# Optimization experiments

Hardware: AMD Instinct MI355X
Metric: run time of the kernel (lower is better)

## Reference

```python
import jax, jax.numpy as jnp
import numpy as np

B, T, DIM, HEADS, KV_HEADS = 2, 2048, 1024, 16, 4
HD = DIM // HEADS  # 64


def _rope(t, sin, cos):
    # interleaved RoPE: pairs (2i, 2i+1) rotated by the same angle
    rot = jnp.stack([-t[..., 1::2], t[..., ::2]], axis=-1).reshape(t.shape)
    return t * cos + rot * sin


def setup_inputs() -> dict:
    key = jax.random.key(0)
    kx, kq, kk, kv, ko = jax.random.split(key, 5)
    x = jax.random.normal(kx, (B, T, DIM), dtype=jnp.float32)
    # standard RoPE tables, [T, HD]
    pos = jnp.arange(T, dtype=jnp.float32)
    inv_freq = 1.0 / (10000.0 ** (jnp.arange(0, HD, 2, dtype=jnp.float32) / HD))
    ang = pos[:, None] * inv_freq[None, :]  # [T, HD/2]
    sin = jnp.repeat(jnp.sin(ang), 2, axis=-1)  # [T, HD]
    cos = jnp.repeat(jnp.cos(ang), 2, axis=-1)
    mask = jnp.ones((B, 1, T), dtype=jnp.float32)  # padding mask (all valid)
    s = 1.0 / np.sqrt(DIM).astype(np.float32)
    Wq = jax.random.normal(kq, (DIM, DIM), dtype=jnp.float32) * s
    Wk = jax.random.normal(kk, (DIM, KV_HEADS * HD), dtype=jnp.float32) * s
    Wv = jax.random.normal(kv, (DIM, KV_HEADS * HD), dtype=jnp.float32) * s
    Wo = jax.random.normal(ko, (DIM, DIM), dtype=jnp.float32) * s
    return {"x": x, "sin": sin, "cos": cos, "mask": mask,
            "Wq": Wq, "Wk": Wk, "Wv": Wv, "Wo": Wo}


def reference(x, sin, cos, mask, Wq, Wk, Wv, Wo):
    Bx, Tx, C = x.shape
    # projections -> [B, H, T, HD] / [B, KV, T, HD]
    q = (x @ Wq).reshape(Bx, Tx, HEADS, HD).transpose(0, 2, 1, 3)
    k = (x @ Wk).reshape(Bx, Tx, KV_HEADS, HD).transpose(0, 2, 1, 3)
    v = (x @ Wv).reshape(Bx, Tx, KV_HEADS, HD).transpose(0, 2, 1, 3)
    # RoPE (sin/cos [T, HD] broadcast over batch/heads)
    q = _rope(q, sin, cos)
    k = _rope(k, sin, cos)
    # GQA: expand kv heads to query heads
    groups = HEADS // KV_HEADS
    k = jnp.repeat(k, groups, axis=1)
    v = jnp.repeat(v, groups, axis=1)
    scores = jnp.einsum('bhqd,bhkd->bhqk', q, k) / np.sqrt(HD).astype(np.float32)
    causal = jnp.tril(jnp.ones((Tx, Tx), dtype=bool))  # [T, T]
    m = (mask[:, None, :, :] > 0) & causal  # [B,1,1,T] & [T,T] -> [B,1,T,T]
    scores = jnp.where(m, scores, jnp.asarray(-1e9, scores.dtype))
    attn = jax.nn.softmax(scores, axis=-1)
    out = jnp.einsum('bhqk,bhkd->bhqd', attn, v)
    out = out.transpose(0, 2, 1, 3).reshape(Bx, Tx, C)
    return out @ Wo
```

## Files before the change

kernel.cpp:

```cpp
#include <hip/hip_runtime.h>
#include <math.h>

typedef __attribute__((ext_vector_type(8))) short bf16x8;
typedef __attribute__((ext_vector_type(4))) float f32x4;
typedef __attribute__((ext_vector_type(4))) unsigned short u16x4;

#define B_    2
#define T_    2048
#define DIM_  1024
#define H_    16
#define KV_   4
#define HD_   64

#define QSCALE 0.1803368801111437f

static __device__ __forceinline__ unsigned short f2bf(float f) {
    union { float f; unsigned int u; } v; v.f = f;
    unsigned int r = v.u + 0x7fff + ((v.u >> 16) & 1);
    return (unsigned short)(r >> 16);
}

static __device__ __forceinline__ unsigned int pkbf(float lo, float hi) {
    union { float f; unsigned int u; } a, b; a.f = lo; b.f = hi;
    return ((a.u + 0x8000u) >> 16) | ((b.u + 0x8000u) & 0xffff0000u);
}

static __device__ __forceinline__ void gload16(const void* g, void* l) {
    __builtin_amdgcn_global_load_lds(
        (const __attribute__((address_space(1))) unsigned int*)g,
        (__attribute__((address_space(3))) unsigned int*)l, 16, 0, 0);
}

#define XB_OFF   0u
#define WT_OFF   4194304u
#define WOT_OFF  5767168u
#define QB_OFF   6815744u
#define KB_OFF   11010048u
#define VTB_OFF  12058624u
#define AB_OFF   13107200u

__global__ __launch_bounds__(256) void cvt_kernel(
    const float* __restrict__ in, unsigned short* __restrict__ out)
{
    const size_t i = ((size_t)blockIdx.x * 256 + threadIdx.x) * 8;
    float4 a = *(const float4*)&in[i];
    float4 b = *(const float4*)&in[i + 4];
    unsigned short u[8] = {f2bf(a.x), f2bf(a.y), f2bf(a.z), f2bf(a.w),
                           f2bf(b.x), f2bf(b.y), f2bf(b.z), f2bf(b.w)};
    *(bf16x8*)&out[i] = *(bf16x8*)u;
}

__global__ __launch_bounds__(256) void wtrans_kernel(
    const float* __restrict__ W, unsigned short* __restrict__ Wt, int N)
{
    __shared__ float Ts[64][65];
    const int n0 = blockIdx.x * 64, k0 = blockIdx.y * 64;
    const int tid = threadIdx.x;
    const int r = tid >> 4, c4 = (tid & 15) * 4;
    #pragma unroll
    for (int i = 0; i < 4; ++i) {
        float4 v = *(const float4*)&W[(size_t)(k0 + r + 16 * i) * N + n0 + c4];
        Ts[r + 16 * i][c4 + 0] = v.x; Ts[r + 16 * i][c4 + 1] = v.y;
        Ts[r + 16 * i][c4 + 2] = v.z; Ts[r + 16 * i][c4 + 3] = v.w;
    }
    __syncthreads();
    const int rn = tid >> 3, ck = (tid & 7) * 8;
    #pragma unroll
    for (int i = 0; i < 2; ++i) {
        int n = rn + 32 * i;
        unsigned short u[8];
        #pragma unroll
        for (int e = 0; e < 8; ++e) u[e] = f2bf(Ts[ck + e][n]);
        *(bf16x8*)&Wt[(size_t)(n0 + n) * 1024 + k0 + ck] = *(bf16x8*)u;
    }
}

__global__ __launch_bounds__(256) void qkv_mfma_kernel(
    const unsigned short* __restrict__ xb, const unsigned short* __restrict__ Wt,
    const float* __restrict__ sinp, const float* __restrict__ cosp,
    unsigned short* __restrict__ Qw, unsigned short* __restrict__ Kw,
    unsigned short* __restrict__ Vtw)
{
    __shared__ __align__(16) unsigned char As[8192];
    __shared__ __align__(16) unsigned char Bs[16384];

    const int tid = threadIdx.x, lane = tid & 63, w = tid >> 6;
    const int lr = lane & 15, lg = lane >> 4;
    const int wm = w >> 1, wn = w & 1;
    const int bn = blockIdx.x, bm = blockIdx.y;
    const int m0 = bm * 64, n0 = bn * 128;

    const int chunkR = lane >> 3;
    const int srcOff = 8 * ((lane & 7) ^ chunkR);

    f32x4 acc[2][4] = {};

    for (int k0 = 0; k0 < 1024; k0 += 64) {
        __syncthreads();
        #pragma unroll
        for (int i = 0; i < 6; ++i) {
            const int c = w * 6 + i;
            if (c < 8) {
                const int row = c * 8 + chunkR;
                gload16(xb + (size_t)(m0 + row) * 1024 + k0 + srcOff, As + c * 1024);
            } else {
                const int row = (c - 8) * 8 + chunkR;
                gload16(Wt + (size_t)(n0 + row) * 1024 + k0 + srcOff,
                        Bs + (c - 8) * 1024);
            }
        }
        __syncthreads();
        #pragma unroll
        for (int kk = 0; kk < 2; ++kk) {
            bf16x8 af[2], bfr[4];
            #pragma unroll
            for (int mf = 0; mf < 2; ++mf) {
                const int row = wm * 32 + mf * 16 + lr;
                af[mf] = *(const bf16x8*)(As + row * 128 +
                          ((kk * 64 + lg * 16) ^ ((row & 7) << 4)));
            }
            #pragma unroll
            for (int nf = 0; nf < 4; ++nf) {
                const int row = wn * 64 + nf * 16 + lr;
                bfr[nf] = *(const bf16x8*)(Bs + row * 128 +
                          ((kk * 64 + lg * 16) ^ ((row & 7) << 4)));
            }
            #pragma unroll
            for (int mf = 0; mf < 2; ++mf)
                #pragma unroll
                for (int nf = 0; nf < 4; ++nf)
                    acc[mf][nf] = __builtin_amdgcn_mfma_f32_16x16x32_bf16(
                        af[mf], bfr[nf], acc[mf][nf], 0, 0, 0);
        }
    }

    const float rsign = (lane & 1) ? 1.f : -1.f;
    #pragma unroll
    for (int nf = 0; nf < 4; ++nf) {
        const int col = n0 + wn * 64 + nf * 16 + lr;
        #pragma unroll
        for (int mf = 0; mf < 2; ++mf) {
            const int mrow = m0 + wm * 32 + mf * 16 + lg * 4;
            const int b = mrow >> 11;
            const int t0 = mrow & 2047;
            if (col < 1280) {
                const int d = col & 63;
                #pragma unroll
                for (int r = 0; r < 4; ++r) {
                    float val = acc[mf][nf][r];
                    float partner = __shfl_xor(val, 1);
                    const int t = t0 + r;
                    float cs = cosp[t * 64 + d], sn = sinp[t * 64 + d];
                    float rv = val * cs + rsign * partner * sn;
                    if (col < 1024) {
                        const int h = col >> 6;
                        Qw[(((size_t)b * H_ + h) * T_ + t) * 64 + d] =
                            f2bf(rv * QSCALE);
                    } else {
                        const int kv = (col - 1024) >> 6;
                        char* krow = (char*)Kw +
                            ((((size_t)b * KV_ + kv) * T_ + t) << 7);
                        *(unsigned short*)(krow + ((2 * d) ^ ((t & 7) << 4))) =
                            f2bf(rv);
                    }
                }
            } else {
                const int cv = col - 1280, kv = cv >> 6, d = cv & 63;
                unsigned short u[4];
                #pragma unroll
                for (int r = 0; r < 4; ++r) u[r] = f2bf(acc[mf][nf][r]);
                char* vrow = (char*)Vtw +
                    ((((size_t)b * KV_ + kv) * 64 + d) * (size_t)T_ * 2);
                *(u16x4*)(vrow + ((2 * t0) ^ ((d & 7) << 4))) = *(u16x4*)u;
            }
        }
    }
}

__global__ __launch_bounds__(512, 4) void attn_kernel(
    const unsigned short* __restrict__ Qg, const unsigned short* __restrict__ Kg,
    const unsigned short* __restrict__ Vtg, const float* __restrict__ maskp,
    unsigned short* __restrict__ attn_out)
{
    __shared__ __align__(16) unsigned char Kl[8192];
    __shared__ __align__(16) unsigned char Vl[8192];
    __shared__ __align__(16) unsigned char Pl[8][2048];
    __shared__ __align__(16) float Ml[2048];

    const int tid  = threadIdx.x;
    const int lane = tid & 63;
    const int w    = tid >> 6;
    const int grp  = w >> 2;
    const int wq   = w & 3;
    const int lr   = lane & 15;
    const int lg   = lane >> 4;

    const int bi   = blockIdx.x;
    const int half = bi >> 8;
    const int j    = bi & 255;
    const int bh   = j >> 3;
    const int idx  = j & 7;
    const int p    = half ? (15 - idx) : idx;
    const int qtA  = 31 - p;
    const int qt   = grp ? p : qtA;
    const int h    = bh & 15;
    const int b    = bh >> 4;
    const int kvh  = h >> 2;
    const int q0   = qt * 64;
    const int qrow = q0 + wq * 16 + lr;

    const char* Kb = (const char*)(Kg  + ((size_t)b * KV_ + kvh) * T_ * HD_);
    const char* Vb = (const char*)(Vtg + ((size_t)b * KV_ + kvh) * HD_ * T_);

    {
        f32x4 mv4 = *(const f32x4*)&maskp[b * T_ + tid * 4];
        f32x4 bv;
        #pragma unroll
        for (int e = 0; e < 4; ++e) bv[e] = mv4[e] > 0.f ? 0.f : -1e30f;
        *(f32x4*)&Ml[tid * 4] = bv;
    }

    const int sr  = lane >> 3;
    const int scb = (lane & 7) * 16;
    unsigned char* Pw = &Pl[w][0];

    const unsigned short* Qbase =
        Qg + (((size_t)b * H_ + h) * T_ + qrow) * HD_;
    const bf16x8 qf0 = *(const bf16x8*)(Qbase + lg * 8);
    const bf16x8 qf1 = *(const bf16x8*)(Qbase + 32 + lg * 8);

    f32x4 o[4] = {};
    float m = -1e30f, l = 0.f;

    for (int kt = 0; kt <= qtA; ++kt) {
        const int k0 = kt * 64;

        {
            const int row = w * 8 + sr;
            gload16(Kb + (size_t)(k0 + row) * 128 + scb, &Kl[w * 1024]);
            gload16(Vb + (size_t)row * 4096 + 2 * k0 + scb, &Vl[w * 1024]);
        }
        __syncthreads();

        if (kt <= qt) {
            f32x4 s[4] = {};
            __builtin_amdgcn_s_setprio(1);
            #pragma unroll
            for (int n = 0; n < 4; ++n) {
                const int key = 16 * n + lr;
                #pragma unroll
                for (int ks = 0; ks < 2; ++ks) {
                    bf16x8 kb = *(const bf16x8*)(Kl +
                        ((key * 128 + 64 * ks + lg * 16) ^ ((key & 7) << 4)));
                    s[n] = __builtin_amdgcn_mfma_f32_16x16x32_bf16(
                        kb, ks == 0 ? qf0 : qf1, s[n], 0, 0, 0);
                }
            }
            __builtin_amdgcn_s_setprio(0);

            if (kt == qt) {
                #pragma unroll
                for (int n = 0; n < 4; ++n) {
                    f32x4 bv = *(const f32x4*)&Ml[k0 + 16 * n + 4 * lg];
                    #pragma unroll
                    for (int r = 0; r < 4; ++r) {
                        const int keyg = k0 + 16 * n + 4 * lg + r;
                        s[n][r] = (keyg <= qrow) ? s[n][r] + bv[r] : -1e30f;
                    }
                }
            } else {
                #pragma unroll
                for (int n = 0; n < 4; ++n) {
                    f32x4 bv = *(const f32x4*)&Ml[k0 + 16 * n + 4 * lg];
                    #pragma unroll
                    for (int r = 0; r < 4; ++r) s[n][r] += bv[r];
                }
            }

            float tmax[4];
            #pragma unroll
            for (int n = 0; n < 4; ++n)
                tmax[n] = fmaxf(fmaxf(s[n][0], s[n][1]), fmaxf(s[n][2], s[n][3]));
            float mx = fmaxf(fmaxf(tmax[0], tmax[1]), fmaxf(tmax[2], tmax[3]));
            mx = fmaxf(mx, __shfl_xor(mx, 16));
            mx = fmaxf(mx, __shfl_xor(mx, 32));
            const float mnew = fmaxf(m, mx);
            const float alpha = exp2f(m - mnew);
            m = mnew;
            #pragma unroll
            for (int n = 0; n < 4; ++n)
                #pragma unroll
                for (int r = 0; r < 4; ++r)
                    s[n][r] = exp2f(s[n][r] - mnew);
            float tsum[4];
            #pragma unroll
            for (int n = 0; n < 4; ++n)
                tsum[n] = (s[n][0] + s[n][1]) + (s[n][2] + s[n][3]);
            float rsum = (tsum[0] + tsum[1]) + (tsum[2] + tsum[3]);
            rsum += __shfl_xor(rsum, 16);
            rsum += __shfl_xor(rsum, 32);
            l = l * alpha + rsum;
            #pragma unroll
            for (int n = 0; n < 4; ++n) o[n] *= alpha;

            #pragma unroll
            for (int n = 0; n < 4; ++n) {
                uint2 wv;
                wv.x = pkbf(s[n][0], s[n][1]);
                wv.y = pkbf(s[n][2], s[n][3]);
                *(uint2*)(Pw + ((lr * 128 + 32 * n + 8 * lg) ^ ((lr & 7) << 4))) = wv;
            }
            bf16x8 pa0 = *(const bf16x8*)(Pw + ((lr * 128 +      lg * 16) ^ ((lr & 7) << 4)));
            bf16x8 pa1 = *(const bf16x8*)(Pw + ((lr * 128 + 64 + lg * 16) ^ ((lr & 7) << 4)));

            __builtin_amdgcn_s_setprio(1);
            #pragma unroll
            for (int n = 0; n < 4; ++n) {
                const int d = 16 * n + lr;
                #pragma unroll
                for (int ks = 0; ks < 2; ++ks) {
                    bf16x8 vb = *(const bf16x8*)(Vl +
                        ((d * 128 + 64 * ks + lg * 16) ^ ((d & 7) << 4)));
                    o[n] = __builtin_amdgcn_mfma_f32_16x16x32_bf16(
                        vb, ks == 0 ? pa0 : pa1, o[n], 0, 0, 0);
                }
            }
            __builtin_amdgcn_s_setprio(0);
        }

        __syncthreads();
    }

    const float linv = 1.f / l;
    unsigned short* orow = attn_out + ((size_t)b * T_ + qrow) * DIM_ + h * HD_;
    #pragma unroll
    for (int n = 0; n < 4; ++n) {
        unsigned short u[4];
        #pragma unroll
        for (int r = 0; r < 4; ++r) u[r] = f2bf(o[n][r] * linv);
        *(u16x4*)&orow[16 * n + 4 * lg] = *(u16x4*)u;
    }
}

__global__ __launch_bounds__(256) void outproj_mfma_kernel(
    const unsigned short* __restrict__ Ab, const unsigned short* __restrict__ Wot,
    float* __restrict__ out)
{
    __shared__ __align__(16) unsigned char As[8192];
    __shared__ __align__(16) unsigned char Bs[16384];

    const int tid = threadIdx.x, lane = tid & 63, w = tid >> 6;
    const int lr = lane & 15, lg = lane >> 4;
    const int wm = w >> 1, wn = w & 1;
    const int bn = blockIdx.x, bm = blockIdx.y;
    const int m0 = bm * 64, n0 = bn * 128;

    const int chunkR = lane >> 3;
    const int srcOff = 8 * ((lane & 7) ^ chunkR);

    f32x4 acc[2][4] = {};

    for (int k0 = 0; k0 < 1024; k0 += 64) {
        __syncthreads();
        #pragma unroll
        for (int i = 0; i < 6; ++i) {
            const int c = w * 6 + i;
            if (c < 8) {
                const int row = c * 8 + chunkR;
                gload16(Ab + (size_t)(m0 + row) * 1024 + k0 + srcOff, As + c * 1024);
            } else {
                const int row = (c - 8) * 8 + chunkR;
                gload16(Wot + (size_t)(n0 + row) * 1024 + k0 + srcOff,
                        Bs + (c - 8) * 1024);
            }
        }
        __syncthreads();
        #pragma unroll
        for (int kk = 0; kk < 2; ++kk) {
            bf16x8 af[2], bfr[4];
            #pragma unroll
            for (int mf = 0; mf < 2; ++mf) {
                const int row = wm * 32 + mf * 16 + lr;
                af[mf] = *(const bf16x8*)(As + row * 128 +
                          ((kk * 64 + lg * 16) ^ ((row & 7) << 4)));
            }
            #pragma unroll
            for (int nf = 0; nf < 4; ++nf) {
                const int row = wn * 64 + nf * 16 + lr;
                bfr[nf] = *(const bf16x8*)(Bs + row * 128 +
                          ((kk * 64 + lg * 16) ^ ((row & 7) << 4)));
            }
            #pragma unroll
            for (int mf = 0; mf < 2; ++mf)
                #pragma unroll
                for (int nf = 0; nf < 4; ++nf)
                    acc[mf][nf] = __builtin_amdgcn_mfma_f32_16x16x32_bf16(
                        af[mf], bfr[nf], acc[mf][nf], 0, 0, 0);
        }
    }

    #pragma unroll
    for (int nf = 0; nf < 4; ++nf) {
        const int col = n0 + wn * 64 + nf * 16 + lr;
        #pragma unroll
        for (int mf = 0; mf < 2; ++mf) {
            const int mrow = m0 + wm * 32 + mf * 16 + lg * 4;
            #pragma unroll
            for (int r = 0; r < 4; ++r)
                out[(size_t)(mrow + r) * 1024 + col] = acc[mf][nf][r];
        }
    }
}

extern "C" void kernel_launch(void* const* d_in, const int* in_sizes, int n_in,
                              void* d_out, int out_size, void* d_ws, size_t ws_size,
                              hipStream_t stream)
{
    const float* x     = (const float*)d_in[0];
    const float* sinp  = (const float*)d_in[1];
    const float* cosp  = (const float*)d_in[2];
    const float* maskp = (const float*)d_in[3];
    const float* Wq    = (const float*)d_in[4];
    const float* Wk    = (const float*)d_in[5];
    const float* Wv    = (const float*)d_in[6];
    const float* Wo    = (const float*)d_in[7];

    unsigned short* wsb = (unsigned short*)d_ws;
    unsigned short* xb  = wsb + XB_OFF;
    unsigned short* Wt  = wsb + WT_OFF;
    unsigned short* Wot = wsb + WOT_OFF;
    unsigned short* Qw  = wsb + QB_OFF;
    unsigned short* Kw  = wsb + KB_OFF;
    unsigned short* Vtw = wsb + VTB_OFF;
    unsigned short* Ab  = wsb + AB_OFF;
    float* out = (float*)d_out;

    cvt_kernel<<<2048, 256, 0, stream>>>(x, xb);
    wtrans_kernel<<<dim3(16, 16), 256, 0, stream>>>(Wq, Wt, 1024);
    wtrans_kernel<<<dim3(4, 16), 256, 0, stream>>>(Wk, Wt + 1024u * 1024u, 256);
    wtrans_kernel<<<dim3(4, 16), 256, 0, stream>>>(Wv, Wt + 1280u * 1024u, 256);
    wtrans_kernel<<<dim3(16, 16), 256, 0, stream>>>(Wo, Wot, 1024);

    qkv_mfma_kernel<<<dim3(12, 64), 256, 0, stream>>>(xb, Wt, sinp, cosp,
                                                      Qw, Kw, Vtw);
    attn_kernel<<<dim3(512), 512, 0, stream>>>(
        Qw, Kw, Vtw, maskp, Ab);
    outproj_mfma_kernel<<<dim3(8, 64), 256, 0, stream>>>(Ab, Wot, out);
}
```

Before: 116.8 us.

## Split KV range between wave groups in attention and merge partial softmax

Each attention block previously paired two query tiles (a causal load-balancing pair) and had both wave groups share one K/V tile per iteration. Now each block handles a single query tile: the two wave groups split its KV tiles into two halves with separate LDS buffers. At the end they merge their partial online-softmax states (m, l, o) through shared memory. The grid doubles to 1024 blocks, ordered heaviest tile first. This raises parallelism and cuts the redundant pairing overhead, at the cost of more LDS, an extra merge step, and idle waves when the halves are uneven.

```diff
diff --git a/kernel.cpp b/kernel.cpp
--- a/kernel.cpp
+++ b/kernel.cpp
@@ -182,9 +182,9 @@
     const unsigned short* __restrict__ Vtg, const float* __restrict__ maskp,
     unsigned short* __restrict__ attn_out)
 {
-    __shared__ __align__(16) unsigned char Kl[8192];
-    __shared__ __align__(16) unsigned char Vl[8192];
-    __shared__ __align__(16) unsigned char Pl[8][2048];
+    __shared__ __align__(16) unsigned char Kl[2][8192];
+    __shared__ __align__(16) unsigned char Vl[2][8192];
+    __shared__ __align__(16) unsigned char Pl[16384];
     __shared__ __align__(16) float Ml[2048];
 
     const int tid  = threadIdx.x;
@@ -196,19 +196,18 @@
     const int lg   = lane >> 4;
 
     const int bi   = blockIdx.x;
-    const int half = bi >> 8;
-    const int j    = bi & 255;
-    const int bh   = j >> 3;
-    const int idx  = j & 7;
-    const int p    = half ? (15 - idx) : idx;
-    const int qtA  = 31 - p;
-    const int qt   = grp ? p : qtA;
+    const int qt   = 31 - (bi >> 5);
+    const int bh   = bi & 31;
     const int h    = bh & 15;
     const int b    = bh >> 4;
     const int kvh  = h >> 2;
     const int q0   = qt * 64;
     const int qrow = q0 + wq * 16 + lr;
 
+    const int nt    = qt + 1;
+    const int mid   = nt >> 1;
+    const int iters = nt - mid;
+
     const char* Kb = (const char*)(Kg  + ((size_t)b * KV_ + kvh) * T_ * HD_);
     const char* Vb = (const char*)(Vtg + ((size_t)b * KV_ + kvh) * HD_ * T_);
 
@@ -222,7 +221,7 @@
 
     const int sr  = lane >> 3;
     const int scb = (lane & 7) * 16;
-    unsigned char* Pw = &Pl[w][0];
+    unsigned char* Pw = &Pl[w * 2048];
 
     const unsigned short* Qbase =
         Qg + (((size_t)b * H_ + h) * T_ + qrow) * HD_;
@@ -232,17 +231,26 @@
     f32x4 o[4] = {};
     float m = -1e30f, l = 0.f;
 
-    for (int kt = 0; kt <= qtA; ++kt) {
-        const int k0 = kt * 64;
-
-        {
-            const int row = w * 8 + sr;
-            gload16(Kb + (size_t)(k0 + row) * 128 + scb, &Kl[w * 1024]);
-            gload16(Vb + (size_t)row * 4096 + 2 * k0 + scb, &Vl[w * 1024]);
-        }
-        __syncthreads();
-
-        if (kt <= qt) {
+    for (int it = 0; it < iters; ++it) {
+        const int ktg = grp ? (mid + it) : it;
+        const bool active = grp || (it < mid);
+        const int k0 = ktg * 64;
+
+        if (active) {
+            #pragma unroll
+            for (int i = 0; i < 2; ++i) {
+                const int rb  = wq * 2 + i;
+                const int row = rb * 8 + sr;
+                gload16(Kb + (size_t)(k0 + row) * 128 + scb, &Kl[grp][rb * 1024]);
+                gload16(Vb + (size_t)row * 4096 + 2 * k0 + scb, &Vl[grp][rb * 1024]);
+            }
+        }
+        __syncthreads();
+
+        if (active) {
+            const unsigned char* Kc = Kl[grp];
+            const unsigned char* Vc = Vl[grp];
+
             f32x4 s[4] = {};
             __builtin_amdgcn_s_setprio(1);
             #pragma unroll
@@ -250,7 +258,7 @@
                 const int key = 16 * n + lr;
                 #pragma unroll
                 for (int ks = 0; ks < 2; ++ks) {
-                    bf16x8 kb = *(const bf16x8*)(Kl +
+                    bf16x8 kb = *(const bf16x8*)(Kc +
                         ((key * 128 + 64 * ks + lg * 16) ^ ((key & 7) << 4)));
                     s[n] = __builtin_amdgcn_mfma_f32_16x16x32_bf16(
                         kb, ks == 0 ? qf0 : qf1, s[n], 0, 0, 0);
@@ -258,7 +266,7 @@
             }
             __builtin_amdgcn_s_setprio(0);
 
-            if (kt == qt) {
+            if (ktg == qt) {
                 #pragma unroll
                 for (int n = 0; n < 4; ++n) {
                     f32x4 bv = *(const f32x4*)&Ml[k0 + 16 * n + 4 * lg];
@@ -319,7 +327,7 @@
                 const int d = 16 * n + lr;
                 #pragma unroll
                 for (int ks = 0; ks < 2; ++ks) {
-                    bf16x8 vb = *(const bf16x8*)(Vl +
+                    bf16x8 vb = *(const bf16x8*)(Vc +
                         ((d * 128 + 64 * ks + lg * 16) ^ ((d & 7) << 4)));
                     o[n] = __builtin_amdgcn_mfma_f32_16x16x32_bf16(
                         vb, ks == 0 ? pa0 : pa1, o[n], 0, 0, 0);
@@ -331,14 +339,34 @@
         __syncthreads();
     }
 
-    const float linv = 1.f / l;
-    unsigned short* orow = attn_out + ((size_t)b * T_ + qrow) * DIM_ + h * HD_;
-    #pragma unroll
-    for (int n = 0; n < 4; ++n) {
-        unsigned short u[4];
-        #pragma unroll
-        for (int r = 0; r < 4; ++r) u[r] = f2bf(o[n][r] * linv);
-        *(u16x4*)&orow[16 * n + 4 * lg] = *(u16x4*)u;
+    const int slot = wq * 64 + lane;
+    if (grp) {
+        float* ob = (float*)Pl;
+        #pragma unroll
+        for (int n = 0; n < 4; ++n)
+            *(f32x4*)&ob[slot * 16 + n * 4] = o[n];
+        Ml[slot]       = m;
+        Ml[256 + slot] = l;
+    }
+    __syncthreads();
+    if (!grp) {
+        const float* ob = (const float*)Pl;
+        const float mB = Ml[slot], lB = Ml[256 + slot];
+        const float ms = fmaxf(m, mB);
+        const float aA = exp2f(m - ms), aB = exp2f(mB - ms);
+        const float lf = l * aA + lB * aB;
+        const float linv = 1.f / lf;
+        unsigned short* orow =
+            attn_out + ((size_t)b * T_ + qrow) * DIM_ + h * HD_;
+        #pragma unroll
+        for (int n = 0; n < 4; ++n) {
+            f32x4 obv = *(const f32x4*)&ob[slot * 16 + n * 4];
+            unsigned short u[4];
+            #pragma unroll
+            for (int r = 0; r < 4; ++r)
+                u[r] = f2bf((o[n][r] * aA + obv[r] * aB) * linv);
+            *(u16x4*)&orow[16 * n + 4 * lg] = *(u16x4*)u;
+        }
     }
 }
 
@@ -443,7 +471,7 @@
 
     qkv_mfma_kernel<<<dim3(12, 64), 256, 0, stream>>>(xb, Wt, sinp, cosp,
                                                       Qw, Kw, Vtw);
-    attn_kernel<<<dim3(512), 512, 0, stream>>>(
+    attn_kernel<<<dim3(1024), 512, 0, stream>>>(
         Qw, Kw, Vtw, maskp, Ab);
     outproj_mfma_kernel<<<dim3(8, 64), 256, 0, stream>>>(Ab, Wot, out);
 }
```

Result: no change. 117.6 us (+0.7%).
